# Performance work log

Hardware: AMD Instinct MI355X
Metric: run time of the kernel (lower is better)

Reference implementation:

```python
import jax, jax.numpy as jnp
import numpy as np

N_NODES = 100000
N_EDGES = 1600000
IN_CH = 128
HIDDEN = 64
HEADS = 4
C = HIDDEN // HEADS  # per-head channels = 16
NEG_SLOPE = 0.2  # PyG GATConv default leaky_relu slope


def setup_inputs() -> dict:
    key = jax.random.key(0)
    ks = jax.random.split(key, 12)
    x = jax.random.normal(ks[0], (N_NODES, IN_CH), dtype=jnp.float32)
    edge_index = jax.random.randint(ks[1], (2, N_EDGES), 0, N_NODES, dtype=jnp.int64)
    s = 0.1
    params = {
        'w1': jax.random.normal(ks[2], (HIDDEN, IN_CH), dtype=jnp.float32) * s,
        'a_src1': jax.random.normal(ks[3], (HEADS, C), dtype=jnp.float32) * s,
        'a_dst1': jax.random.normal(ks[4], (HEADS, C), dtype=jnp.float32) * s,
        'b1': jax.random.normal(ks[5], (HIDDEN,), dtype=jnp.float32) * s,
        'w2': jax.random.normal(ks[6], (HIDDEN, HIDDEN), dtype=jnp.float32) * s,
        'a_src2': jax.random.normal(ks[7], (HEADS, C), dtype=jnp.float32) * s,
        'a_dst2': jax.random.normal(ks[8], (HEADS, C), dtype=jnp.float32) * s,
        'b2': jax.random.normal(ks[9], (HIDDEN,), dtype=jnp.float32) * s,
        'fc_w': jax.random.normal(ks[10], (1, HIDDEN), dtype=jnp.float32) * s,
        'fc_b': jax.random.normal(ks[11], (1,), dtype=jnp.float32) * s,
    }
    return {'x': x, 'edge_index': edge_index, **params}


def _gat_layer(x, src, dst, W, a_src, a_dst, b):
    # x: [N, F_in]; src/dst: [E'] (self-loops already appended)
    N = x.shape[0]
    h = (x @ W.T).reshape(N, HEADS, C)                      # [N, H, C]
    e_src = jnp.einsum('nhc,hc->nh', h, a_src)              # [N, H]
    e_dst = jnp.einsum('nhc,hc->nh', h, a_dst)              # [N, H]
    alpha = jax.nn.leaky_relu(e_src[src] + e_dst[dst], NEG_SLOPE)  # [E', H]
    # segment softmax over incoming edges of each dst node
    amax = jax.ops.segment_max(alpha, dst, num_segments=N)  # [N, H]
    alpha = jnp.exp(alpha - amax[dst])
    denom = jax.ops.segment_sum(alpha, dst, num_segments=N)
    alpha = alpha / (denom[dst] + 1e-16)
    msg = h[src] * alpha[:, :, None]                        # [E', H, C]
    out = jax.ops.segment_sum(msg, dst, num_segments=N)     # [N, H, C]
    return out.reshape(N, HEADS * C) + b


def _forward(x, edge_index, w1, a_src1, a_dst1, b1, w2, a_src2, a_dst2, b2, fc_w, fc_b):
    N = x.shape[0]
    loops = jnp.arange(N, dtype=edge_index.dtype)
    src = jnp.concatenate([edge_index[0], loops])  # PyG GATConv add_self_loops=True
    dst = jnp.concatenate([edge_index[1], loops])
    x = jax.nn.elu(_gat_layer(x, src, dst, w1, a_src1, a_dst1, b1))
    x = jax.nn.elu(_gat_layer(x, src, dst, w2, a_src2, a_dst2, b2))
    return x @ fc_w.T + fc_b  # [N, 1]


def reference(x, edge_index, w1, a_src1, a_dst1, b1, w2, a_src2, a_dst2, b2, fc_w, fc_b):
    return _forward(x, edge_index, w1, a_src1, a_dst1, b1, w2, a_src2, a_dst2, b2, fc_w, fc_b)
```

## Files before the change

### kernel.cpp

```cpp
#include <hip/hip_runtime.h>
#include <hip/hip_fp16.h>
#include <math.h>

#define NEG_SLOPE 0.2f
#define BSH 8
#define CAPB 6144

__device__ __forceinline__ float lrelu(float x) { return x > 0.f ? x : NEG_SLOPE * x; }

using half4 = __attribute__((ext_vector_type(4))) _Float16;
using half8 = __attribute__((ext_vector_type(8))) _Float16;
using f32x4 = __attribute__((ext_vector_type(4))) float;

template <typename TIn>
__device__ __forceinline__ float4 ld4(const TIn* p);
template <>
__device__ __forceinline__ float4 ld4<float>(const float* p) { return *(const float4*)p; }
template <>
__device__ __forceinline__ float4 ld4<_Float16>(const _Float16* p) {
    half4 v = *(const half4*)p;
    return make_float4((float)v[0], (float)v[1], (float)v[2], (float)v[3]);
}

template <int K, typename TIn>
__device__ __forceinline__ void gemm_mfma_body(const TIn* __restrict__ x,
                                               const float* __restrict__ W,
                                               const float* __restrict__ a_src,
                                               const float* __restrict__ a_dst,
                                               unsigned short* __restrict__ h_f16,
                                               float* __restrict__ es,
                                               float* __restrict__ ed,
                                               int N, int bid, _Float16* sm) {
    constexpr int KP = K + 8;
    _Float16* xs = sm;
    _Float16* ws = sm + 64 * KP;
    const int tid = threadIdx.x;
    const int n0 = bid * 64;

    constexpr int KV = K / 4;
    for (int idx = tid; idx < 64 * KV; idx += 256) {
        int r = idx / KV, kq = idx - r * KV;
        int n = n0 + r;
        float4 v = (n < N) ? ld4<TIn>(x + (size_t)n * K + kq * 4)
                           : make_float4(0.f, 0.f, 0.f, 0.f);
        half4 hv = {(_Float16)v.x, (_Float16)v.y, (_Float16)v.z, (_Float16)v.w};
        *(half4*)&xs[r * KP + kq * 4] = hv;
        float4 wv = *(const float4*)(W + (size_t)r * K + kq * 4);
        half4 wh = {(_Float16)wv.x, (_Float16)wv.y, (_Float16)wv.z, (_Float16)wv.w};
        *(half4*)&ws[r * KP + kq * 4] = wh;
    }
    __syncthreads();

    const int wv_ = tid >> 6, lane = tid & 63;
    const int lrow = lane & 15, g = lane >> 4;
    f32x4 acc0 = {0.f, 0.f, 0.f, 0.f}, acc1 = acc0, acc2 = acc0, acc3 = acc0;
#pragma unroll
    for (int ks = 0; ks < K / 32; ++ks) {
        const int ko = ks * 32 + g * 8;
        half8 af = *(const half8*)&xs[(wv_ * 16 + lrow) * KP + ko];
        half8 b0 = *(const half8*)&ws[(lrow) * KP + ko];
        half8 b1 = *(const half8*)&ws[(16 + lrow) * KP + ko];
        half8 b2 = *(const half8*)&ws[(32 + lrow) * KP + ko];
        half8 b3 = *(const half8*)&ws[(48 + lrow) * KP + ko];
        acc0 = __builtin_amdgcn_mfma_f32_16x16x32_f16(af, b0, acc0, 0, 0, 0);
        acc1 = __builtin_amdgcn_mfma_f32_16x16x32_f16(af, b1, acc1, 0, 0, 0);
        acc2 = __builtin_amdgcn_mfma_f32_16x16x32_f16(af, b2, acc2, 0, 0, 0);
        acc3 = __builtin_amdgcn_mfma_f32_16x16x32_f16(af, b3, acc3, 0, 0, 0);
    }
    __syncthreads();

    _Float16* ht = sm;
#pragma unroll
    for (int reg = 0; reg < 4; ++reg) {
        int r = wv_ * 16 + g * 4 + reg;
        ht[r * 72 +      lrow] = (_Float16)acc0[reg];
        ht[r * 72 + 16 + lrow] = (_Float16)acc1[reg];
        ht[r * 72 + 32 + lrow] = (_Float16)acc2[reg];
        ht[r * 72 + 48 + lrow] = (_Float16)acc3[reg];
    }
    __syncthreads();

    {
        int nl = tid >> 2, hd = tid & 3;
        half8 hA = *(const half8*)&ht[nl * 72 + hd * 16];
        half8 hB = *(const half8*)&ht[nl * 72 + hd * 16 + 8];
        const float4 s0 = *(const float4*)(a_src + hd * 16);
        const float4 s1 = *(const float4*)(a_src + hd * 16 + 4);
        const float4 s2 = *(const float4*)(a_src + hd * 16 + 8);
        const float4 s3 = *(const float4*)(a_src + hd * 16 + 12);
        const float4 d0 = *(const float4*)(a_dst + hd * 16);
        const float4 d1 = *(const float4*)(a_dst + hd * 16 + 4);
        const float4 d2 = *(const float4*)(a_dst + hd * 16 + 8);
        const float4 d3 = *(const float4*)(a_dst + hd * 16 + 12);
        float e1 = (float)hA[0]*s0.x + (float)hA[1]*s0.y + (float)hA[2]*s0.z + (float)hA[3]*s0.w
                 + (float)hA[4]*s1.x + (float)hA[5]*s1.y + (float)hA[6]*s1.z + (float)hA[7]*s1.w
                 + (float)hB[0]*s2.x + (float)hB[1]*s2.y + (float)hB[2]*s2.z + (float)hB[3]*s2.w
                 + (float)hB[4]*s3.x + (float)hB[5]*s3.y + (float)hB[6]*s3.z + (float)hB[7]*s3.w;
        float e2 = (float)hA[0]*d0.x + (float)hA[1]*d0.y + (float)hA[2]*d0.z + (float)hA[3]*d0.w
                 + (float)hA[4]*d1.x + (float)hA[5]*d1.y + (float)hA[6]*d1.z + (float)hA[7]*d1.w
                 + (float)hB[0]*d2.x + (float)hB[1]*d2.y + (float)hB[2]*d2.z + (float)hB[3]*d2.w
                 + (float)hB[4]*d3.x + (float)hB[5]*d3.y + (float)hB[6]*d3.z + (float)hB[7]*d3.w;
        int n = n0 + nl;
        if (n < N) {
            es[(size_t)n * 4 + hd] = e1;
            ed[(size_t)n * 4 + hd] = e2;
        }
    }
    for (int idx = tid; idx < 512; idx += 256) {
        int r = idx >> 3, c8 = (idx & 7) << 3;
        if (n0 + r < N)
            *(uint4*)(h_f16 + (size_t)(n0 + r) * 64 + c8) = *(const uint4*)&ht[r * 72 + c8];
    }
}

template <int K>
__global__ __launch_bounds__(256) void gemm1_hist(const float* __restrict__ x,
                                                  const float* __restrict__ W,
                                                  const float* __restrict__ a_src,
                                                  const float* __restrict__ a_dst,
                                                  unsigned short* __restrict__ h_f16,
                                                  float* __restrict__ es,
                                                  float* __restrict__ ed, int N,
                                                  const int* __restrict__ dst,
                                                  int* __restrict__ hist_g,
                                                  int E, int Etot, int NBUCK, int nIter,
                                                  int NH) {
    __shared__ _Float16 sm[2 * 64 * (K + 8)];
    if ((int)blockIdx.x < NH) {
        int* hist = (int*)sm;
        int blk = blockIdx.x, tid = threadIdx.x;
        for (int i = tid; i < NBUCK; i += 256) hist[i] = 0;
        __syncthreads();
        int base = blk * nIter * 256;
        for (int i = 0; i < nIter; ++i) {
            int e = base + i * 256 + tid;
            if (e < Etot) {
                int d = (e < E) ? dst[e] : e - E;
                atomicAdd(&hist[d >> BSH], 1);
            }
        }
        __syncthreads();
        for (int i = tid; i < NBUCK; i += 256) hist_g[(size_t)blk * NBUCK + i] = hist[i];
        return;
    }
    gemm_mfma_body<K, float>(x, W, a_src, a_dst, h_f16, es, ed, N, blockIdx.x - NH, sm);
}

template <int K, typename TIn>
__global__ __launch_bounds__(256) void gemm_mfma(const TIn* __restrict__ x,
                                                 const float* __restrict__ W,
                                                 const float* __restrict__ a_src,
                                                 const float* __restrict__ a_dst,
                                                 unsigned short* __restrict__ h_f16,
                                                 float* __restrict__ es,
                                                 float* __restrict__ ed, int N) {
    __shared__ _Float16 sm[2 * 64 * (K + 8)];
    gemm_mfma_body<K, TIn>(x, W, a_src, a_dst, h_f16, es, ed, N, blockIdx.x, sm);
}

__global__ __launch_bounds__(256) void bucket_scan_blocks(int* __restrict__ hist_g,
                                                          int* __restrict__ tot,
                                                          int NBUCK, int NBLK) {
    __shared__ int s[256];
    int b = blockIdx.x, tid = threadIdx.x;
    int v = (tid < NBLK) ? hist_g[(size_t)tid * NBUCK + b] : 0;
    s[tid] = v; __syncthreads();
#pragma unroll
    for (int off = 1; off < 256; off <<= 1) {
        int t = (tid >= off) ? s[tid - off] : 0;
        __syncthreads();
        s[tid] += t;
        __syncthreads();
    }
    if (tid < NBLK) hist_g[(size_t)tid * NBUCK + b] = s[tid] - v;
    if (tid == 255) tot[b] = s[255];
}

__device__ __forceinline__ void local_tot_scan(const int* __restrict__ tot, int* sv, int NBUCK) {
    int tid = threadIdx.x;
    sv[tid]       = (tid < NBUCK)       ? tot[tid]       : 0;
    sv[tid + 256] = (tid + 256 < NBUCK) ? tot[tid + 256] : 0;
    __syncthreads();
#pragma unroll
    for (int off = 1; off < 512; off <<= 1) {
        int a1 = (tid >= off) ? sv[tid - off] : 0;
        int a2 = (tid + 256 >= off) ? sv[tid + 256 - off] : 0;
        __syncthreads();
        sv[tid] += a1; sv[tid + 256] += a2;
        __syncthreads();
    }
}

__global__ __launch_bounds__(256) void bucket_scatter(const int* __restrict__ src,
                                                      const int* __restrict__ dst,
                                                      const int* __restrict__ hist_g,
                                                      const int* __restrict__ tot,
                                                      unsigned int* __restrict__ bbuf,
                                                      int E, int Etot, int NBUCK, int nIter) {
    __shared__ int sv[512];
    __shared__ int lcur[512];
    int blk = blockIdx.x, tid = threadIdx.x;
    local_tot_scan(tot, sv, NBUCK);
    for (int i = tid; i < NBUCK; i += 256)
        lcur[i] = (sv[i] - tot[i]) + hist_g[(size_t)blk * NBUCK + i];
    __syncthreads();
    int base = blk * nIter * 256;
    for (int i = 0; i < nIter; ++i) {
        int e = base + i * 256 + tid;
        if (e >= Etot) continue;
        int s, d;
        if (e < E) { s = src[e]; d = dst[e]; } else { s = d = e - E; }
        int pos = atomicAdd(&lcur[d >> BSH], 1);
        bbuf[pos] = (unsigned)s | ((unsigned)(d & ((1 << BSH) - 1)) << 24);
    }
}

__global__ __launch_bounds__(256) void bucket_build(const unsigned int* __restrict__ bbuf,
                                                    const int* __restrict__ tot,
                                                    int* __restrict__ col,
                                                    int* __restrict__ offs,
                                                    int N, int NBUCK, int Etot) {
    __shared__ int sv[512];
    __shared__ int cnt[256], lcur[256], s[256];
    __shared__ int ordered[CAPB];
    int b = blockIdx.x, tid = threadIdx.x;
    local_tot_scan(tot, sv, NBUCK);
    const int t  = tot[b];
    const int bb = sv[b] - t;
    const int n0 = b << BSH;
    if (b == 0 && tid == 0) offs[N] = Etot;
    cnt[tid] = 0;
    __syncthreads();
    for (int i = tid; i < t; i += 256) {
        unsigned v = bbuf[bb + i];
        atomicAdd(&cnt[v >> 24], 1);
    }
    __syncthreads();
    int c = cnt[tid];
    s[tid] = c; __syncthreads();
#pragma unroll
    for (int off = 1; off < 256; off <<= 1) {
        int tt = (tid >= off) ? s[tid - off] : 0;
        __syncthreads();
        s[tid] += tt;
        __syncthreads();
    }
    int ex = s[tid] - c;
    lcur[tid] = ex;
    if (n0 + tid < N) offs[n0 + tid] = bb + ex;
    __syncthreads();
    if (t <= CAPB) {
        for (int i = tid; i < t; i += 256) {
            unsigned v = bbuf[bb + i];
            int pos = atomicAdd(&lcur[v >> 24], 1);
            ordered[pos] = (int)(v & 0xFFFFFFu);
        }
        __syncthreads();
        for (int i = tid; i < t; i += 256) col[bb + i] = ordered[i];
    } else {
        for (int i = tid; i < t; i += 256) {
            unsigned v = bbuf[bb + i];
            int pos = atomicAdd(&lcur[v >> 24], 1);
            col[bb + pos] = (int)(v & 0xFFFFFFu);
        }
    }
}

template <int D>
__device__ __forceinline__ void batch2n(int myCol, int cm1, int cnt32, int half,
                                        int eslot, int co, int hd, float edv,
                                        const float* __restrict__ es,
                                        const unsigned short* __restrict__ h_f16,
                                        float* acc, float& l) {
    int   sidx[D];
    float ev[D];
    uint4 hv[D];
#pragma unroll
    for (int d = 0; d < D; ++d)
        sidx[d] = __shfl(myCol, (half << 5) + min(eslot + 4 * d, cm1), 64);
#pragma unroll
    for (int d = 0; d < D; ++d)
        ev[d] = es[(size_t)sidx[d] * 4 + hd];
#pragma unroll
    for (int d = 0; d < D; ++d)
        hv[d] = *(const uint4*)(h_f16 + (size_t)sidx[d] * 64 + co * 8);
    float p[D];
#pragma unroll
    for (int d = 0; d < D; ++d)
        p[d] = (eslot + 4 * d < cnt32) ? __expf(lrelu(ev[d] + edv)) : 0.f;
#pragma unroll
    for (int d = 0; d < D; ++d) {
        union { uint4 u; __half h[8]; } u;
        u.u = hv[d];
        acc[0] += p[d] * __half2float(u.h[0]); acc[1] += p[d] * __half2float(u.h[1]);
        acc[2] += p[d] * __half2float(u.h[2]); acc[3] += p[d] * __half2float(u.h[3]);
        acc[4] += p[d] * __half2float(u.h[4]); acc[5] += p[d] * __half2float(u.h[5]);
        acc[6] += p[d] * __half2float(u.h[6]); acc[7] += p[d] * __half2float(u.h[7]);
        l += p[d];
    }
}

template <bool FINAL>
__global__ __launch_bounds__(256) void gat_gather2n(const int* __restrict__ offs,
                                                    const int* __restrict__ col,
                                                    const float* __restrict__ es,
                                                    const float* __restrict__ ed,
                                                    const unsigned short* __restrict__ h_f16,
                                                    const float* __restrict__ b,
                                                    const float* __restrict__ fcw,
                                                    const float* __restrict__ fcb,
                                                    float* __restrict__ xo,
                                                    unsigned short* __restrict__ xo_h,
                                                    int N) {
    const int pair = (blockIdx.x * 256 + threadIdx.x) >> 6;
    const int lane = threadIdx.x & 63;
    const int half = lane >> 5, ll = lane & 31;
    const int eslot = ll >> 3, co = ll & 7, hd = co >> 1;
    const int w = pair * 2 + half;
    const bool vnode = w < N;

    int beg = 0, cnt = 1;
    if (vnode) { beg = offs[w]; cnt = offs[w + 1] - beg; }
    const float edv = vnode ? ed[(size_t)w * 4 + hd] : 0.f;

    const int cnt32 = min(cnt, 32);
    const int cm1 = cnt32 - 1;
    int myCol = col[beg + min(ll, cm1)];
    int mcnt = max(cnt, __shfl_xor(cnt, 32, 64));

    float acc[8] = {0.f, 0.f, 0.f, 0.f, 0.f, 0.f, 0.f, 0.f};
    float l = 0.f;

    const int mcnt32 = min(mcnt, 32);
    if (mcnt32 <= 8) {
        batch2n<2>(myCol, cm1, cnt32, half, eslot, co, hd, edv, es, h_f16, acc, l);
    } else if (mcnt32 <= 16) {
        batch2n<4>(myCol, cm1, cnt32, half, eslot, co, hd, edv, es, h_f16, acc, l);
    } else if (mcnt32 <= 24) {
        batch2n<6>(myCol, cm1, cnt32, half, eslot, co, hd, edv, es, h_f16, acc, l);
    } else {
        batch2n<8>(myCol, cm1, cnt32, half, eslot, co, hd, edv, es, h_f16, acc, l);
        for (int j = 32; j < mcnt; j += 4) {
            int k = j + eslot;
            bool valid = k < cnt;
            int s = valid ? col[beg + k] : 0;
            float a = es[(size_t)s * 4 + hd] + edv;
            float p = valid ? __expf(lrelu(a)) : 0.f;
            union { uint4 u; __half h[8]; } hv;
            hv.u = *(const uint4*)(h_f16 + (size_t)s * 64 + co * 8);
            acc[0] += p * __half2float(hv.h[0]); acc[1] += p * __half2float(hv.h[1]);
            acc[2] += p * __half2float(hv.h[2]); acc[3] += p * __half2float(hv.h[3]);
            acc[4] += p * __half2float(hv.h[4]); acc[5] += p * __half2float(hv.h[5]);
            acc[6] += p * __half2float(hv.h[6]); acc[7] += p * __half2float(hv.h[7]);
            l += p;
        }
    }

#pragma unroll
    for (int m = 8; m <= 16; m <<= 1) {
#pragma unroll
        for (int q = 0; q < 8; ++q) acc[q] += __shfl_xor(acc[q], m, 64);
        l += __shfl_xor(l, m, 64);
    }
    const float inv = 1.f / (l + 1e-16f);
    const float4 bv0 = *(const float4*)(b + co * 8);
    const float4 bv1 = *(const float4*)(b + co * 8 + 4);
    float v0 = acc[0] * inv + bv0.x, v1 = acc[1] * inv + bv0.y;
    float v2 = acc[2] * inv + bv0.z, v3 = acc[3] * inv + bv0.w;
    float v4 = acc[4] * inv + bv1.x, v5 = acc[5] * inv + bv1.y;
    float v6 = acc[6] * inv + bv1.z, v7 = acc[7] * inv + bv1.w;
    v0 = v0 > 0.f ? v0 : __expf(v0) - 1.f;
    v1 = v1 > 0.f ? v1 : __expf(v1) - 1.f;
    v2 = v2 > 0.f ? v2 : __expf(v2) - 1.f;
    v3 = v3 > 0.f ? v3 : __expf(v3) - 1.f;
    v4 = v4 > 0.f ? v4 : __expf(v4) - 1.f;
    v5 = v5 > 0.f ? v5 : __expf(v5) - 1.f;
    v6 = v6 > 0.f ? v6 : __expf(v6) - 1.f;
    v7 = v7 > 0.f ? v7 : __expf(v7) - 1.f;
    if (FINAL) {
        const float4 fw0 = *(const float4*)(fcw + co * 8);
        const float4 fw1 = *(const float4*)(fcw + co * 8 + 4);
        float t = v0 * fw0.x + v1 * fw0.y + v2 * fw0.z + v3 * fw0.w +
                  v4 * fw1.x + v5 * fw1.y + v6 * fw1.z + v7 * fw1.w;
#pragma unroll
        for (int m = 1; m <= 4; m <<= 1) t += __shfl_xor(t, m, 64);
        if (ll == 0 && vnode) xo[w] = t + fcb[0];
    } else {
        if (ll < 8 && vnode) {
            unsigned p0u = (unsigned)__half_as_ushort(__float2half_rn(v0)) |
                           ((unsigned)__half_as_ushort(__float2half_rn(v1)) << 16);
            unsigned p1u = (unsigned)__half_as_ushort(__float2half_rn(v2)) |
                           ((unsigned)__half_as_ushort(__float2half_rn(v3)) << 16);
            unsigned p2u = (unsigned)__half_as_ushort(__float2half_rn(v4)) |
                           ((unsigned)__half_as_ushort(__float2half_rn(v5)) << 16);
            unsigned p3u = (unsigned)__half_as_ushort(__float2half_rn(v6)) |
                           ((unsigned)__half_as_ushort(__float2half_rn(v7)) << 16);
            *(uint4*)(xo_h + (size_t)w * 64 + co * 8) = make_uint4(p0u, p1u, p2u, p3u);
        }
    }
}

extern "C" void kernel_launch(void* const* d_in, const int* in_sizes, int n_in,
                              void* d_out, int out_size, void* d_ws, size_t ws_size,
                              hipStream_t stream) {
    const float* x   = (const float*)d_in[0];
    const int*   ei  = (const int*)d_in[1];
    const float* w1  = (const float*)d_in[2];
    const float* as1 = (const float*)d_in[3];
    const float* ad1 = (const float*)d_in[4];
    const float* b1  = (const float*)d_in[5];
    const float* w2  = (const float*)d_in[6];
    const float* as2 = (const float*)d_in[7];
    const float* ad2 = (const float*)d_in[8];
    const float* b2  = (const float*)d_in[9];
    const float* fcw = (const float*)d_in[10];
    const float* fcb = (const float*)d_in[11];
    float* out = (float*)d_out;

    const int N = in_sizes[0] / 128;
    const int E = in_sizes[1] / 2;
    const int Etot = E + N;
    const int* src = ei;
    const int* dst = ei + E;

    const int NBUCK = (N + 255) >> BSH;
    int CHe = 8192;
    while ((Etot + CHe - 1) / CHe > 256) CHe *= 2;
    const int NBLK = (Etot + CHe - 1) / CHe;
    const int nIter = CHe / 256;

    char* p = (char*)d_ws;
    unsigned short* h_f16 = (unsigned short*)p;  p += (size_t)N * 64 * 2;
    unsigned short* x2    = (unsigned short*)p;  p += (size_t)N * 64 * 2;
    float* es    = (float*)p;  p += (size_t)N * 4 * 4;
    float* ed    = (float*)p;  p += (size_t)N * 4 * 4;
    int* offs    = (int*)p;    p += (size_t)(N + 1) * 4;
    int* tot     = (int*)p;    p += (size_t)NBUCK * 4;
    int* hist_g  = (int*)p;    p += (size_t)NBLK * NBUCK * 4;
    int* col     = (int*)p;    p += (size_t)Etot * 4;
    unsigned int* bbuf = (unsigned int*)p;  p += (size_t)Etot * 4;

    dim3 blk(256);
    const int gN64t = (N + 63) / 64;
    const int nPair = (N + 1) / 2;
    const int gW2   = (nPair * 64 + 255) / 256;

    gemm1_hist<128><<<NBLK + gN64t, blk, 0, stream>>>(x, w1, as1, ad1, h_f16, es, ed, N,
                                                      dst, hist_g, E, Etot, NBUCK, nIter, NBLK);
    bucket_scan_blocks<<<NBUCK, blk, 0, stream>>>(hist_g, tot, NBUCK, NBLK);
    bucket_scatter<<<NBLK, blk, 0, stream>>>(src, dst, hist_g, tot, bbuf, E, Etot, NBUCK, nIter);
    bucket_build<<<NBUCK, blk, 0, stream>>>(bbuf, tot, col, offs, N, NBUCK, Etot);

    gat_gather2n<false><<<gW2, blk, 0, stream>>>(offs, col, es, ed, h_f16, b1,
                                                 nullptr, nullptr, nullptr, x2, N);
    gemm_mfma<64, _Float16><<<gN64t, blk, 0, stream>>>((const _Float16*)x2, w2, as2, ad2,
                                                       h_f16, es, ed, N);
    gat_gather2n<true><<<gW2, blk, 0, stream>>>(offs, col, es, ed, h_f16, b2,
                                                fcw, fcb, out, nullptr, N);
}
```

Before: 150.6 us.

## Fuse layer-1 aggregation with layer-2 GEMM into one kernel

Layer-1 neighbor aggregation and the layer-2 projection GEMM now run in a single kernel. Each 64-node block gathers its rows into shared memory as fp16 and then runs the MFMA GEMM and attention-score epilogue directly. This drops one launch and the global write and read of the intermediate x2 buffer. In exchange, each block processes its 64 nodes in eight sequential gather passes per wave before the GEMM. Separate h/es/ed buffers per layer avoid read/write hazards.

```diff
diff --git a/kernel.cpp b/kernel.cpp
--- a/kernel.cpp
+++ b/kernel.cpp
@@ -22,64 +22,14 @@
     return make_float4((float)v[0], (float)v[1], (float)v[2], (float)v[3]);
 }
 
-template <int K, typename TIn>
-__device__ __forceinline__ void gemm_mfma_body(const TIn* __restrict__ x,
-                                               const float* __restrict__ W,
-                                               const float* __restrict__ a_src,
-                                               const float* __restrict__ a_dst,
-                                               unsigned short* __restrict__ h_f16,
-                                               float* __restrict__ es,
-                                               float* __restrict__ ed,
-                                               int N, int bid, _Float16* sm) {
-    constexpr int KP = K + 8;
-    _Float16* xs = sm;
-    _Float16* ws = sm + 64 * KP;
+__device__ __forceinline__ void gemm_epilogue(const _Float16* ht,
+                                              const float* __restrict__ a_src,
+                                              const float* __restrict__ a_dst,
+                                              unsigned short* __restrict__ h_f16,
+                                              float* __restrict__ es,
+                                              float* __restrict__ ed,
+                                              int N, int n0) {
     const int tid = threadIdx.x;
-    const int n0 = bid * 64;
-
-    constexpr int KV = K / 4;
-    for (int idx = tid; idx < 64 * KV; idx += 256) {
-        int r = idx / KV, kq = idx - r * KV;
-        int n = n0 + r;
-        float4 v = (n < N) ? ld4<TIn>(x + (size_t)n * K + kq * 4)
-                           : make_float4(0.f, 0.f, 0.f, 0.f);
-        half4 hv = {(_Float16)v.x, (_Float16)v.y, (_Float16)v.z, (_Float16)v.w};
-        *(half4*)&xs[r * KP + kq * 4] = hv;
-        float4 wv = *(const float4*)(W + (size_t)r * K + kq * 4);
-        half4 wh = {(_Float16)wv.x, (_Float16)wv.y, (_Float16)wv.z, (_Float16)wv.w};
-        *(half4*)&ws[r * KP + kq * 4] = wh;
-    }
-    __syncthreads();
-
-    const int wv_ = tid >> 6, lane = tid & 63;
-    const int lrow = lane & 15, g = lane >> 4;
-    f32x4 acc0 = {0.f, 0.f, 0.f, 0.f}, acc1 = acc0, acc2 = acc0, acc3 = acc0;
-#pragma unroll
-    for (int ks = 0; ks < K / 32; ++ks) {
-        const int ko = ks * 32 + g * 8;
-        half8 af = *(const half8*)&xs[(wv_ * 16 + lrow) * KP + ko];
-        half8 b0 = *(const half8*)&ws[(lrow) * KP + ko];
-        half8 b1 = *(const half8*)&ws[(16 + lrow) * KP + ko];
-        half8 b2 = *(const half8*)&ws[(32 + lrow) * KP + ko];
-        half8 b3 = *(const half8*)&ws[(48 + lrow) * KP + ko];
-        acc0 = __builtin_amdgcn_mfma_f32_16x16x32_f16(af, b0, acc0, 0, 0, 0);
-        acc1 = __builtin_amdgcn_mfma_f32_16x16x32_f16(af, b1, acc1, 0, 0, 0);
-        acc2 = __builtin_amdgcn_mfma_f32_16x16x32_f16(af, b2, acc2, 0, 0, 0);
-        acc3 = __builtin_amdgcn_mfma_f32_16x16x32_f16(af, b3, acc3, 0, 0, 0);
-    }
-    __syncthreads();
-
-    _Float16* ht = sm;
-#pragma unroll
-    for (int reg = 0; reg < 4; ++reg) {
-        int r = wv_ * 16 + g * 4 + reg;
-        ht[r * 72 +      lrow] = (_Float16)acc0[reg];
-        ht[r * 72 + 16 + lrow] = (_Float16)acc1[reg];
-        ht[r * 72 + 32 + lrow] = (_Float16)acc2[reg];
-        ht[r * 72 + 48 + lrow] = (_Float16)acc3[reg];
-    }
-    __syncthreads();
-
     {
         int nl = tid >> 2, hd = tid & 3;
         half8 hA = *(const half8*)&ht[nl * 72 + hd * 16];
@@ -113,6 +63,66 @@
     }
 }
 
+template <int K, typename TIn>
+__device__ __forceinline__ void gemm_mfma_body(const TIn* __restrict__ x,
+                                               const float* __restrict__ W,
+                                               const float* __restrict__ a_src,
+                                               const float* __restrict__ a_dst,
+                                               unsigned short* __restrict__ h_f16,
+                                               float* __restrict__ es,
+                                               float* __restrict__ ed,
+                                               int N, int bid, _Float16* sm) {
+    constexpr int KP = K + 8;
+    _Float16* xs = sm;
+    _Float16* ws = sm + 64 * KP;
+    const int tid = threadIdx.x;
+    const int n0 = bid * 64;
+
+    constexpr int KV = K / 4;
+    for (int idx = tid; idx < 64 * KV; idx += 256) {
+        int r = idx / KV, kq = idx - r * KV;
+        int n = n0 + r;
+        float4 v = (n < N) ? ld4<TIn>(x + (size_t)n * K + kq * 4)
+                           : make_float4(0.f, 0.f, 0.f, 0.f);
+        half4 hv = {(_Float16)v.x, (_Float16)v.y, (_Float16)v.z, (_Float16)v.w};
+        *(half4*)&xs[r * KP + kq * 4] = hv;
+        float4 wv = *(const float4*)(W + (size_t)r * K + kq * 4);
+        half4 wh = {(_Float16)wv.x, (_Float16)wv.y, (_Float16)wv.z, (_Float16)wv.w};
+        *(half4*)&ws[r * KP + kq * 4] = wh;
+    }
+    __syncthreads();
+
+    const int wv_ = tid >> 6, lane = tid & 63;
+    const int lrow = lane & 15, g = lane >> 4;
+    f32x4 acc0 = {0.f, 0.f, 0.f, 0.f}, acc1 = acc0, acc2 = acc0, acc3 = acc0;
+#pragma unroll
+    for (int ks = 0; ks < K / 32; ++ks) {
+        const int ko = ks * 32 + g * 8;
+        half8 af = *(const half8*)&xs[(wv_ * 16 + lrow) * KP + ko];
+        half8 b0 = *(const half8*)&ws[(lrow) * KP + ko];
+        half8 b1 = *(const half8*)&ws[(16 + lrow) * KP + ko];
+        half8 b2 = *(const half8*)&ws[(32 + lrow) * KP + ko];
+        half8 b3 = *(const half8*)&ws[(48 + lrow) * KP + ko];
+        acc0 = __builtin_amdgcn_mfma_f32_16x16x32_f16(af, b0, acc0, 0, 0, 0);
+        acc1 = __builtin_amdgcn_mfma_f32_16x16x32_f16(af, b1, acc1, 0, 0, 0);
+        acc2 = __builtin_amdgcn_mfma_f32_16x16x32_f16(af, b2, acc2, 0, 0, 0);
+        acc3 = __builtin_amdgcn_mfma_f32_16x16x32_f16(af, b3, acc3, 0, 0, 0);
+    }
+    __syncthreads();
+
+    _Float16* ht = sm;
+#pragma unroll
+    for (int reg = 0; reg < 4; ++reg) {
+        int r = wv_ * 16 + g * 4 + reg;
+        ht[r * 72 +      lrow] = (_Float16)acc0[reg];
+        ht[r * 72 + 16 + lrow] = (_Float16)acc1[reg];
+        ht[r * 72 + 32 + lrow] = (_Float16)acc2[reg];
+        ht[r * 72 + 48 + lrow] = (_Float16)acc3[reg];
+    }
+    __syncthreads();
+    gemm_epilogue(ht, a_src, a_dst, h_f16, es, ed, N, n0);
+}
+
 template <int K>
 __global__ __launch_bounds__(256) void gemm1_hist(const float* __restrict__ x,
                                                   const float* __restrict__ W,
@@ -146,18 +156,6 @@
     gemm_mfma_body<K, float>(x, W, a_src, a_dst, h_f16, es, ed, N, blockIdx.x - NH, sm);
 }
 
-template <int K, typename TIn>
-__global__ __launch_bounds__(256) void gemm_mfma(const TIn* __restrict__ x,
-                                                 const float* __restrict__ W,
-                                                 const float* __restrict__ a_src,
-                                                 const float* __restrict__ a_dst,
-                                                 unsigned short* __restrict__ h_f16,
-                                                 float* __restrict__ es,
-                                                 float* __restrict__ ed, int N) {
-    __shared__ _Float16 sm[2 * 64 * (K + 8)];
-    gemm_mfma_body<K, TIn>(x, W, a_src, a_dst, h_f16, es, ed, N, blockIdx.x, sm);
-}
-
 __global__ __launch_bounds__(256) void bucket_scan_blocks(int* __restrict__ hist_g,
                                                           int* __restrict__ tot,
                                                           int NBUCK, int NBLK) {
@@ -300,25 +298,15 @@
     }
 }
 
-template <bool FINAL>
-__global__ __launch_bounds__(256) void gat_gather2n(const int* __restrict__ offs,
-                                                    const int* __restrict__ col,
-                                                    const float* __restrict__ es,
-                                                    const float* __restrict__ ed,
-                                                    const unsigned short* __restrict__ h_f16,
-                                                    const float* __restrict__ b,
-                                                    const float* __restrict__ fcw,
-                                                    const float* __restrict__ fcb,
-                                                    float* __restrict__ xo,
-                                                    unsigned short* __restrict__ xo_h,
-                                                    int N) {
-    const int pair = (blockIdx.x * 256 + threadIdx.x) >> 6;
-    const int lane = threadIdx.x & 63;
-    const int half = lane >> 5, ll = lane & 31;
-    const int eslot = ll >> 3, co = ll & 7, hd = co >> 1;
-    const int w = pair * 2 + half;
-    const bool vnode = w < N;
-
+__device__ __forceinline__ void gather_pair(int w, bool vnode, int half, int eslot,
+                                            int co, int hd, int ll,
+                                            const int* __restrict__ offs,
+                                            const int* __restrict__ col,
+                                            const float* __restrict__ es,
+                                            const float* __restrict__ ed,
+                                            const unsigned short* __restrict__ h_f16,
+                                            const float* __restrict__ b,
+                                            float* v) {
     int beg = 0, cnt = 1;
     if (vnode) { beg = offs[w]; cnt = offs[w + 1] - beg; }
     const float edv = vnode ? ed[(size_t)w * 4 + hd] : 0.f;
@@ -365,39 +353,122 @@
     const float inv = 1.f / (l + 1e-16f);
     const float4 bv0 = *(const float4*)(b + co * 8);
     const float4 bv1 = *(const float4*)(b + co * 8 + 4);
-    float v0 = acc[0] * inv + bv0.x, v1 = acc[1] * inv + bv0.y;
-    float v2 = acc[2] * inv + bv0.z, v3 = acc[3] * inv + bv0.w;
-    float v4 = acc[4] * inv + bv1.x, v5 = acc[5] * inv + bv1.y;
-    float v6 = acc[6] * inv + bv1.z, v7 = acc[7] * inv + bv1.w;
-    v0 = v0 > 0.f ? v0 : __expf(v0) - 1.f;
-    v1 = v1 > 0.f ? v1 : __expf(v1) - 1.f;
-    v2 = v2 > 0.f ? v2 : __expf(v2) - 1.f;
-    v3 = v3 > 0.f ? v3 : __expf(v3) - 1.f;
-    v4 = v4 > 0.f ? v4 : __expf(v4) - 1.f;
-    v5 = v5 > 0.f ? v5 : __expf(v5) - 1.f;
-    v6 = v6 > 0.f ? v6 : __expf(v6) - 1.f;
-    v7 = v7 > 0.f ? v7 : __expf(v7) - 1.f;
-    if (FINAL) {
-        const float4 fw0 = *(const float4*)(fcw + co * 8);
-        const float4 fw1 = *(const float4*)(fcw + co * 8 + 4);
-        float t = v0 * fw0.x + v1 * fw0.y + v2 * fw0.z + v3 * fw0.w +
-                  v4 * fw1.x + v5 * fw1.y + v6 * fw1.z + v7 * fw1.w;
-#pragma unroll
-        for (int m = 1; m <= 4; m <<= 1) t += __shfl_xor(t, m, 64);
-        if (ll == 0 && vnode) xo[w] = t + fcb[0];
-    } else {
-        if (ll < 8 && vnode) {
-            unsigned p0u = (unsigned)__half_as_ushort(__float2half_rn(v0)) |
-                           ((unsigned)__half_as_ushort(__float2half_rn(v1)) << 16);
-            unsigned p1u = (unsigned)__half_as_ushort(__float2half_rn(v2)) |
-                           ((unsigned)__half_as_ushort(__float2half_rn(v3)) << 16);
-            unsigned p2u = (unsigned)__half_as_ushort(__float2half_rn(v4)) |
-                           ((unsigned)__half_as_ushort(__float2half_rn(v5)) << 16);
-            unsigned p3u = (unsigned)__half_as_ushort(__float2half_rn(v6)) |
-                           ((unsigned)__half_as_ushort(__float2half_rn(v7)) << 16);
-            *(uint4*)(xo_h + (size_t)w * 64 + co * 8) = make_uint4(p0u, p1u, p2u, p3u);
+    v[0] = acc[0] * inv + bv0.x; v[1] = acc[1] * inv + bv0.y;
+    v[2] = acc[2] * inv + bv0.z; v[3] = acc[3] * inv + bv0.w;
+    v[4] = acc[4] * inv + bv1.x; v[5] = acc[5] * inv + bv1.y;
+    v[6] = acc[6] * inv + bv1.z; v[7] = acc[7] * inv + bv1.w;
+#pragma unroll
+    for (int q = 0; q < 8; ++q) v[q] = v[q] > 0.f ? v[q] : __expf(v[q]) - 1.f;
+}
+
+__global__ __launch_bounds__(256) void gather1_gemm2(const int* __restrict__ offs,
+                                                     const int* __restrict__ col,
+                                                     const float* __restrict__ es1,
+                                                     const float* __restrict__ ed1,
+                                                     const unsigned short* __restrict__ h1,
+                                                     const float* __restrict__ b1,
+                                                     const float* __restrict__ W2,
+                                                     const float* __restrict__ as2,
+                                                     const float* __restrict__ ad2,
+                                                     unsigned short* __restrict__ h2,
+                                                     float* __restrict__ es2,
+                                                     float* __restrict__ ed2,
+                                                     int N) {
+    __shared__ _Float16 sm[2 * 64 * 72];
+    _Float16* x2t = sm;
+    _Float16* ws  = sm + 64 * 72;
+    const int tid = threadIdx.x;
+    const int n0 = blockIdx.x * 64;
+    const int wv_ = tid >> 6, lane = tid & 63;
+    const int half = lane >> 5, ll = lane & 31;
+    const int eslot = ll >> 3, co = ll & 7, hd = co >> 1;
+
+    for (int idx = tid; idx < 64 * 16; idx += 256) {
+        int r = idx >> 4, kq = idx & 15;
+        float4 wv4 = *(const float4*)(W2 + (size_t)r * 64 + kq * 4);
+        half4 wh = {(_Float16)wv4.x, (_Float16)wv4.y, (_Float16)wv4.z, (_Float16)wv4.w};
+        *(half4*)&ws[r * 72 + kq * 4] = wh;
+    }
+
+    for (int pass = 0; pass < 8; ++pass) {
+        int lr = wv_ * 16 + pass * 2 + half;
+        int w = n0 + lr;
+        bool vnode = w < N;
+        float v[8];
+        gather_pair(w, vnode, half, eslot, co, hd, ll, offs, col, es1, ed1, h1, b1, v);
+        if (ll < 8) {
+            uint4 pk = make_uint4(0u, 0u, 0u, 0u);
+            if (vnode) {
+                pk.x = (unsigned)__half_as_ushort(__float2half_rn(v[0])) |
+                       ((unsigned)__half_as_ushort(__float2half_rn(v[1])) << 16);
+                pk.y = (unsigned)__half_as_ushort(__float2half_rn(v[2])) |
+                       ((unsigned)__half_as_ushort(__float2half_rn(v[3])) << 16);
+                pk.z = (unsigned)__half_as_ushort(__float2half_rn(v[4])) |
+                       ((unsigned)__half_as_ushort(__float2half_rn(v[5])) << 16);
+                pk.w = (unsigned)__half_as_ushort(__float2half_rn(v[6])) |
+                       ((unsigned)__half_as_ushort(__float2half_rn(v[7])) << 16);
+            }
+            *(uint4*)&x2t[lr * 72 + co * 8] = pk;
         }
     }
+    __syncthreads();
+
+    const int lrow = lane & 15, g = lane >> 4;
+    f32x4 acc0 = {0.f, 0.f, 0.f, 0.f}, acc1 = acc0, acc2 = acc0, acc3 = acc0;
+#pragma unroll
+    for (int ks = 0; ks < 2; ++ks) {
+        const int ko = ks * 32 + g * 8;
+        half8 af = *(const half8*)&x2t[(wv_ * 16 + lrow) * 72 + ko];
+        half8 b0 = *(const half8*)&ws[(lrow) * 72 + ko];
+        half8 b1v = *(const half8*)&ws[(16 + lrow) * 72 + ko];
+        half8 b2v = *(const half8*)&ws[(32 + lrow) * 72 + ko];
+        half8 b3v = *(const half8*)&ws[(48 + lrow) * 72 + ko];
+        acc0 = __builtin_amdgcn_mfma_f32_16x16x32_f16(af, b0, acc0, 0, 0, 0);
+        acc1 = __builtin_amdgcn_mfma_f32_16x16x32_f16(af, b1v, acc1, 0, 0, 0);
+        acc2 = __builtin_amdgcn_mfma_f32_16x16x32_f16(af, b2v, acc2, 0, 0, 0);
+        acc3 = __builtin_amdgcn_mfma_f32_16x16x32_f16(af, b3v, acc3, 0, 0, 0);
+    }
+    __syncthreads();
+
+    _Float16* ht = sm;
+#pragma unroll
+    for (int reg = 0; reg < 4; ++reg) {
+        int r = wv_ * 16 + g * 4 + reg;
+        ht[r * 72 +      lrow] = (_Float16)acc0[reg];
+        ht[r * 72 + 16 + lrow] = (_Float16)acc1[reg];
+        ht[r * 72 + 32 + lrow] = (_Float16)acc2[reg];
+        ht[r * 72 + 48 + lrow] = (_Float16)acc3[reg];
+    }
+    __syncthreads();
+    gemm_epilogue(ht, as2, ad2, h2, es2, ed2, N, n0);
+}
+
+__global__ __launch_bounds__(256) void gat_final(const int* __restrict__ offs,
+                                                 const int* __restrict__ col,
+                                                 const float* __restrict__ es,
+                                                 const float* __restrict__ ed,
+                                                 const unsigned short* __restrict__ h_f16,
+                                                 const float* __restrict__ b,
+                                                 const float* __restrict__ fcw,
+                                                 const float* __restrict__ fcb,
+                                                 float* __restrict__ xo, int N) {
+    const int pair = (blockIdx.x * 256 + threadIdx.x) >> 6;
+    const int lane = threadIdx.x & 63;
+    const int half = lane >> 5, ll = lane & 31;
+    const int eslot = ll >> 3, co = ll & 7, hd = co >> 1;
+    const int w = pair * 2 + half;
+    const bool vnode = w < N;
+
+    float v[8];
+    gather_pair(w, vnode, half, eslot, co, hd, ll, offs, col, es, ed, h_f16, b, v);
+
+    const float4 fw0 = *(const float4*)(fcw + co * 8);
+    const float4 fw1 = *(const float4*)(fcw + co * 8 + 4);
+    float t = v[0] * fw0.x + v[1] * fw0.y + v[2] * fw0.z + v[3] * fw0.w +
+              v[4] * fw1.x + v[5] * fw1.y + v[6] * fw1.z + v[7] * fw1.w;
+#pragma unroll
+    for (int m = 1; m <= 4; m <<= 1) t += __shfl_xor(t, m, 64);
+    if (ll == 0 && vnode) xo[w] = t + fcb[0];
 }
 
 extern "C" void kernel_launch(void* const* d_in, const int* in_sizes, int n_in,
@@ -430,10 +501,12 @@
     const int nIter = CHe / 256;
 
     char* p = (char*)d_ws;
-    unsigned short* h_f16 = (unsigned short*)p;  p += (size_t)N * 64 * 2;
-    unsigned short* x2    = (unsigned short*)p;  p += (size_t)N * 64 * 2;
-    float* es    = (float*)p;  p += (size_t)N * 4 * 4;
-    float* ed    = (float*)p;  p += (size_t)N * 4 * 4;
+    unsigned short* h1 = (unsigned short*)p;  p += (size_t)N * 64 * 2;
+    unsigned short* h2 = (unsigned short*)p;  p += (size_t)N * 64 * 2;
+    float* es1   = (float*)p;  p += (size_t)N * 4 * 4;
+    float* ed1   = (float*)p;  p += (size_t)N * 4 * 4;
+    float* es2   = (float*)p;  p += (size_t)N * 4 * 4;
+    float* ed2   = (float*)p;  p += (size_t)N * 4 * 4;
     int* offs    = (int*)p;    p += (size_t)(N + 1) * 4;
     int* tot     = (int*)p;    p += (size_t)NBUCK * 4;
     int* hist_g  = (int*)p;    p += (size_t)NBLK * NBUCK * 4;
@@ -445,16 +518,13 @@
     const int nPair = (N + 1) / 2;
     const int gW2   = (nPair * 64 + 255) / 256;
 
-    gemm1_hist<128><<<NBLK + gN64t, blk, 0, stream>>>(x, w1, as1, ad1, h_f16, es, ed, N,
+    gemm1_hist<128><<<NBLK + gN64t, blk, 0, stream>>>(x, w1, as1, ad1, h1, es1, ed1, N,
                                                       dst, hist_g, E, Etot, NBUCK, nIter, NBLK);
     bucket_scan_blocks<<<NBUCK, blk, 0, stream>>>(hist_g, tot, NBUCK, NBLK);
     bucket_scatter<<<NBLK, blk, 0, stream>>>(src, dst, hist_g, tot, bbuf, E, Etot, NBUCK, nIter);
     bucket_build<<<NBUCK, blk, 0, stream>>>(bbuf, tot, col, offs, N, NBUCK, Etot);
 
-    gat_gather2n<false><<<gW2, blk, 0, stream>>>(offs, col, es, ed, h_f16, b1,
-                                                 nullptr, nullptr, nullptr, x2, N);
-    gemm_mfma<64, _Float16><<<gN64t, blk, 0, stream>>>((const _Float16*)x2, w2, as2, ad2,
-                                                       h_f16, es, ed, N);
-    gat_gather2n<true><<<gW2, blk, 0, stream>>>(offs, col, es, ed, h_f16, b2,
-                                                fcw, fcb, out, nullptr, N);
-}
+    gather1_gemm2<<<gN64t, blk, 0, stream>>>(offs, col, es1, ed1, h1, b1,
+                                             w2, as2, ad2, h2, es2, ed2, N);
+    gat_final<<<gW2, blk, 0, stream>>>(offs, col, es2, ed2, h2, b2, fcw, fcb, out, N);
+}
```

Measured after the change: 154.2 us. 1.02x slower.
